# Kernel tuning notes

Hardware: AMD Instinct MI355X
Metric: run time of the kernel (lower is better)

## Reference

```python
import jax, jax.numpy as jnp
import numpy as np

# Expert output sizes per answer type: yes/no, number, other (VQA v2)
SIZES = [2, 482, 3129]
MAX_ANS = max(SIZES)  # 3129, padded output width
D_IN = 1024
D_HID = 1000
BATCH = 16384
N_TYPES = len(SIZES)


def setup_inputs() -> dict:
    key = jax.random.key(0)
    ks = jax.random.split(key, 2 + 4 * N_TYPES)
    inp = {
        "hidden_states": jax.random.normal(ks[0], (BATCH, D_IN), dtype=jnp.float32),
        "question_type_output": jax.random.normal(ks[1], (BATCH, N_TYPES), dtype=jnp.float32),
    }
    # Learned params for each expert MLP: Linear(1024->1000), Tanh, Linear(1000->n_e)
    for e, n_out in enumerate(SIZES):
        k1, k2, k3, k4 = ks[2 + 4 * e], ks[3 + 4 * e], ks[4 + 4 * e], ks[5 + 4 * e]
        inp[f"w1_{e}"] = jax.random.normal(k1, (D_IN, D_HID), dtype=jnp.float32) * 0.02
        inp[f"b1_{e}"] = jax.random.normal(k2, (D_HID,), dtype=jnp.float32) * 0.02
        inp[f"w2_{e}"] = jax.random.normal(k3, (D_HID, n_out), dtype=jnp.float32) * 0.02
        inp[f"b2_{e}"] = jax.random.normal(k4, (n_out,), dtype=jnp.float32) * 0.02
    return inp


def _expert(x, w1, b1, w2, b2):
    # Linear -> Dropout(eval: identity) -> Tanh -> Linear
    return jnp.tanh(x @ w1 + b1) @ w2 + b2


def reference(hidden_states, question_type_output,
              w1_0, b1_0, w2_0, b2_0,
              w1_1, b1_1, w2_1, b2_1,
              w1_2, b1_2, w2_2, b2_2):
    params = [(w1_0, b1_0, w2_0, b2_0),
              (w1_1, b1_1, w2_1, b2_1),
              (w1_2, b1_2, w2_2, b2_2)]
    # Route each sample to the expert of its argmax question type.
    pred = jnp.argmax(question_type_output, axis=1)  # [B] int
    out = jnp.zeros((hidden_states.shape[0], MAX_ANS), dtype=hidden_states.dtype)
    # Small fixed loop over N_TYPES experts (structurally distinct weights);
    # each expert runs batched over all samples, then a mask selects routed rows.
    for e, (w1, b1, w2, b2) in enumerate(params):
        o = _expert(hidden_states, w1, b1, w2, b2)          # [B, n_e]
        o = jnp.pad(o, ((0, 0), (0, MAX_ANS - o.shape[1])))  # zero-pad to [B, MAX]
        out = jnp.where((pred == e)[:, None], o, out)
    return out
```

## Files before the change

### kernel.cpp

```cpp
#include <hip/hip_runtime.h>

typedef __attribute__((ext_vector_type(8))) __bf16 bf16x8;
typedef __attribute__((ext_vector_type(4))) float f32x4;

constexpr int BATCH = 16384;
constexpr int DIN   = 1024;
constexpr int DHID  = 1000;
constexpr int MAXA  = 3129;
constexpr int MBMAX = 131;

constexpr size_t SZ_AP  = (size_t)MBMAX * 32 * 8192;
constexpr size_t SZ_HP  = SZ_AP;
constexpr size_t SZ_W1P = 3 * 8 * 32 * 8192;
constexpr size_t SZ_W2P = 30 * 32 * 8192;
constexpr size_t WS_HP  = 0;
constexpr size_t WS_W1P = WS_HP + SZ_HP;
constexpr size_t WS_W2P = WS_W1P + SZ_W1P;
constexpr size_t WS_CNT = WS_W2P + SZ_W2P;
constexpr size_t WS_IDX = WS_CNT + 1024;
constexpr size_t WS_AP  = WS_IDX + 3 * BATCH * 4;
constexpr size_t WS_NEED = WS_AP + SZ_AP;

constexpr int PA_BLK = 2096;
constexpr int PW1_BLK = 1536;
constexpr int PW2_BLK = 1920;

__device__ __forceinline__ ushort f2bf(float f) {
    return __builtin_bit_cast(ushort, (__bf16)f);
}

__device__ __forceinline__ void gload16(const void* g, void* l) {
    __builtin_amdgcn_global_load_lds((const __attribute__((address_space(1))) void*)g,
                                     (__attribute__((address_space(3))) void*)l, 16, 0, 0);
}

__global__ void zero_k(int* __restrict__ c) { if (threadIdx.x < 16) c[threadIdx.x] = 0; }

__global__ void route_k(const float* __restrict__ qt, int* __restrict__ counts,
                        int* __restrict__ idx) {
    int i = blockIdx.x * 256 + threadIdx.x;
    if (i >= BATCH) return;
    float a = qt[3 * i], b = qt[3 * i + 1], c = qt[3 * i + 2];
    int p = 0; float m = a;
    if (b > m) { m = b; p = 1; }
    if (c > m) { m = c; p = 2; }
    int pos = atomicAdd(&counts[p], 1);
    idx[p * BATCH + pos] = i;
}

__global__ void pack_all_k(const float* __restrict__ hs,
                           const float* __restrict__ w1_0, const float* __restrict__ w1_1,
                           const float* __restrict__ w1_2,
                           const float* __restrict__ w2_0, const float* __restrict__ w2_1,
                           const float* __restrict__ w2_2,
                           const int* __restrict__ counts, const int* __restrict__ idx,
                           ushort* __restrict__ Ap, ushort* __restrict__ W1p,
                           ushort* __restrict__ W2p) {
    const int b = blockIdx.x, tid = threadIdx.x;
    if (b < PA_BLK) {
        const int g = b * 256 + tid;
        const int m = g & 127, kt = (g >> 7) & 31, mb = g >> 12;
        const int c0 = counts[0], c1 = counts[1], c2 = counts[2];
        const int n0 = (c0 + 127) >> 7, n1 = (c1 + 127) >> 7, n2 = (c2 + 127) >> 7;
        if (mb >= n0 + n1 + n2) return;
        int e = 0, lm = mb, cnt = c0;
        if (lm >= n0) { lm -= n0; e = 1; cnt = c1; }
        if (e == 1 && lm >= n1) { lm -= n1; e = 2; cnt = c2; }
        int ri = lm * 128 + m; if (ri >= cnt) ri = cnt - 1;
        const float* row = hs + (size_t)idx[e * BATCH + ri] * DIN + kt * 32;
        ushort* dst = Ap + (size_t)(mb * 32 + kt) * 4096 + m * 8;
#pragma unroll
        for (int kc = 0; kc < 4; kc++) {
            float4 f0 = *reinterpret_cast<const float4*>(row + kc * 8);
            float4 f1 = *reinterpret_cast<const float4*>(row + kc * 8 + 4);
            union { ushort u[8]; int4 v; } p;
            p.u[0] = f2bf(f0.x); p.u[1] = f2bf(f0.y); p.u[2] = f2bf(f0.z); p.u[3] = f2bf(f0.w);
            p.u[4] = f2bf(f1.x); p.u[5] = f2bf(f1.y); p.u[6] = f2bf(f1.z); p.u[7] = f2bf(f1.w);
            *reinterpret_cast<int4*>(dst + kc * 1024) = p.v;
        }
    } else if (b < PA_BLK + PW1_BLK) {
        const int g = (b - PA_BLK) * 256 + tid;
        const int n = g & 127, kc = (g >> 7) & 3, kt = (g >> 9) & 31, nb = (g >> 14) & 7, e = g >> 17;
        const float* W = e == 0 ? w1_0 : e == 1 ? w1_1 : w1_2;
        const int nn = nb * 128 + n;
        union { ushort u[8]; int4 v; } p;
#pragma unroll
        for (int j = 0; j < 8; j++) {
            int k = kt * 32 + kc * 8 + j;
            float f = (nn < DHID) ? W[(size_t)k * DHID + nn] : 0.f;
            p.u[j] = f2bf(f);
        }
        *reinterpret_cast<int4*>(W1p + ((size_t)((e * 8 + nb) * 32 + kt)) * 4096 + (kc * 128 + n) * 8) = p.v;
    } else {
        const int g = (b - PA_BLK - PW1_BLK) * 256 + tid;
        const int n = g & 127, kc = (g >> 7) & 3, kt = (g >> 9) & 31, t = g >> 14;
        const int e = (t < 1) ? 0 : (t < 5) ? 1 : 2;
        const int nb = t - (e == 0 ? 0 : e == 1 ? 1 : 5);
        const int ne = e == 0 ? 2 : e == 1 ? 482 : MAXA;
        const float* W = e == 0 ? w2_0 : e == 1 ? w2_1 : w2_2;
        const int nn = nb * 128 + n;
        union { ushort u[8]; int4 v; } p;
#pragma unroll
        for (int j = 0; j < 8; j++) {
            int k = kt * 32 + kc * 8 + j;
            float f = (k < DHID && nn < ne) ? W[(size_t)k * ne + nn] : 0.f;
            p.u[j] = f2bf(f);
        }
        *reinterpret_cast<int4*>(W2p + ((size_t)(t * 32 + kt)) * 4096 + (kc * 128 + n) * 8) = p.v;
    }
}

#define STAGE(BUFO, KT)                                                         \
    {                                                                           \
        const char* as_ = Ag + (size_t)(KT) * 8192 + tid * 16;                  \
        gload16(as_, lds + (BUFO) + w * 1024);                                  \
        const char* bs_ = Bg + (size_t)(KT) * 8192 + tid * 16;                  \
        gload16(bs_, lds + (BUFO) + 8192 + w * 1024);                           \
    }

#define KLOOP()                                                                 \
    f32x4 acc[2][4] = {};                                                       \
    STAGE(0, 0)                                                                 \
    STAGE(16384, 1)                                                             \
    {                                                                           \
        int cur = 0;                                                            \
        for (int kt = 0; kt < 32; ++kt) {                                       \
            if (kt < 31) asm volatile("s_waitcnt vmcnt(2)" ::: "memory");       \
            else         asm volatile("s_waitcnt vmcnt(0)" ::: "memory");       \
            asm volatile("s_barrier" ::: "memory");                             \
            if (kt + 2 < 32) {                                                  \
                int nx = cur + 2; if (nx >= 3) nx -= 3;                         \
                STAGE(nx * 16384, kt + 2)                                       \
            }                                                                   \
            const char* base = lds + cur * 16384;                               \
            bf16x8 af[2], bfr[4];                                               \
            _Pragma("unroll")                                                   \
            for (int mi = 0; mi < 2; mi++)                                      \
                af[mi] = *reinterpret_cast<const bf16x8*>(                      \
                    base + kq4 * 2048 + (wm * 32 + mi * 16 + l15) * 16);        \
            _Pragma("unroll")                                                   \
            for (int ni = 0; ni < 4; ni++)                                      \
                bfr[ni] = *reinterpret_cast<const bf16x8*>(                     \
                    base + 8192 + kq4 * 2048 + (wn * 64 + ni * 16 + l15) * 16); \
            __builtin_amdgcn_s_setprio(1);                                      \
            _Pragma("unroll")                                                   \
            for (int mi = 0; mi < 2; mi++)                                      \
                _Pragma("unroll")                                               \
                for (int ni = 0; ni < 4; ni++)                                  \
                    acc[mi][ni] = __builtin_amdgcn_mfma_f32_16x16x32_bf16(      \
                        af[mi], bfr[ni], acc[mi][ni], 0, 0, 0);                 \
            __builtin_amdgcn_s_setprio(0);                                      \
            cur = cur + 1; if (cur == 3) cur = 0;                               \
        }                                                                       \
    }                                                                           \
    asm volatile("s_barrier" ::: "memory");

__global__ __launch_bounds__(512, 3)
void gemm1_k(const char* __restrict__ ApB, const char* __restrict__ W1pB,
             const float* __restrict__ b1_0, const float* __restrict__ b1_1,
             const float* __restrict__ b1_2,
             const int* __restrict__ counts, int* __restrict__ wq,
             char* __restrict__ HpB) {
    __shared__ __align__(16) char lds[49152];
    __shared__ int s_t;
    const int c0 = counts[0], c1 = counts[1], c2 = counts[2];
    const int n0 = (c0 + 127) >> 7, n1 = (c1 + 127) >> 7, n2 = (c2 + 127) >> 7;
    const int T = (n0 + n1 + n2) * 8;

    const int tid = threadIdx.x;
    const int lane = tid & 63, w = tid >> 6;
    const int wm = w >> 1, wn = w & 1;
    const int l15 = lane & 15, kq4 = lane >> 4;

    for (;;) {
        if (tid == 0) s_t = atomicAdd(wq, 1);
        __syncthreads();
        const int t = s_t;
        if (t >= T) break;

        const int mbG = t >> 3, nbk = t & 7;
        int e = 0, lm = mbG;
        if (lm >= n0) { lm -= n0; e = 1; }
        if (e == 1 && lm >= n1) { lm -= n1; e = 2; }
        const float* bias = e == 0 ? b1_0 : e == 1 ? b1_1 : b1_2;
        const char* Ag = ApB + (size_t)mbG * (32 * 8192);
        const char* Bg = W1pB + (size_t)((e * 8 + nbk) * 32) * 8192;

        KLOOP()

        ushort* img = (ushort*)lds;
#pragma unroll
        for (int mi = 0; mi < 2; mi++) {
            const int rb = wm * 32 + mi * 16 + kq4 * 4;
#pragma unroll
            for (int ni = 0; ni < 4; ni++) {
                const int nl = wn * 64 + ni * 16 + l15;
                const int ng = nbk * 128 + nl;
                const bool live = ng < DHID;
                const float bv = live ? bias[ng] : 0.f;
                const int ua = ((nl >> 5) * 4096 + ((nl >> 3) & 3) * 1024 + (nl & 6)) & ~1;
#pragma unroll
                for (int rg = 0; rg < 4; rg++) {
                    float vv = live ? tanhf(acc[mi][ni][rg] + bv) : 0.f;
                    float vo = __shfl_xor(vv, 1);
                    ushort lo = (l15 & 1) ? f2bf(vo) : f2bf(vv);
                    ushort hi = (l15 & 1) ? f2bf(vv) : f2bf(vo);
                    *reinterpret_cast<uint*>(img + ua + (rb + rg) * 8) =
                        (uint)lo | ((uint)hi << 16);
                }
            }
        }
        asm volatile("s_barrier" ::: "memory");
        char* hdst = HpB + ((size_t)mbG * 32 + nbk * 4) * 8192;
#pragma unroll
        for (int i2 = 0; i2 < 4; i2++) {
            const int s = tid + i2 * 512;
            *reinterpret_cast<int4*>(hdst + s * 16) =
                *reinterpret_cast<const int4*>(lds + s * 16);
        }
        asm volatile("s_barrier" ::: "memory");
    }
}

__global__ __launch_bounds__(512, 3)
void gemm2_k(const char* __restrict__ HpB, const char* __restrict__ W2pB,
             const float* __restrict__ b2_0, const float* __restrict__ b2_1,
             const float* __restrict__ b2_2,
             const int* __restrict__ counts, const int* __restrict__ idx,
             int* __restrict__ wq, int fallback, float* __restrict__ Out) {
    __shared__ __align__(16) char lds[49152];
    __shared__ int s_t;
    const int c0 = counts[0], c1 = counts[1], c2 = counts[2];
    int nb[3]  = {(c0 + 127) >> 7, (c1 + 127) >> 7, (c2 + 127) >> 7};
    int cc[3]  = {c0, c1, c2};
    const int nbn[3]  = {1, 4, 25};
    const int nz[3]   = {24, 21, 0};
    const int zst[3]  = {128, 512, 0};
    const int toff[3] = {0, 1, 5};
    const int nel[3]  = {2, 482, MAXA};
    const int Tc = nb[0] * 1 + nb[1] * 4 + nb[2] * 25;
    const int Tz = fallback ? (nb[0] * 24 + nb[1] * 21) : 0;
    const int T = Tc + Tz;

    const int tid = threadIdx.x;
    const int lane = tid & 63, w = tid >> 6;
    const int wm = w >> 1, wn = w & 1;
    const int l15 = lane & 15, kq4 = lane >> 4;

    for (;;) {
        if (tid == 0) s_t = atomicAdd(wq, 1);
        __syncthreads();
        const int t = s_t;
        if (t >= T) break;

        if (t < Tc) {
            int e = 0, r = t, mbG = 0;
            while (e < 2 && r >= nb[e] * nbn[e]) { r -= nb[e] * nbn[e]; mbG += nb[e]; ++e; }
            const int lm = r / nbn[e], nbk = r - lm * nbn[e];
            mbG += lm;
            const int cnt = cc[e], ne = nel[e];
            const float* bias = e == 0 ? b2_0 : e == 1 ? b2_1 : b2_2;
            const char* Ag = HpB + (size_t)mbG * (32 * 8192);
            const char* Bg = W2pB + (size_t)((toff[e] + nbk) * 32) * 8192;

            KLOOP()

            const int m0 = lm * 128;
            float* bf32 = (float*)lds;
            const int* ip = idx + e * BATCH;
#pragma unroll
            for (int h = 0; h < 2; h++) {
                if ((wm >> 1) == h) {
#pragma unroll
                    for (int mi = 0; mi < 2; mi++) {
                        const int rl = (wm & 1) * 32 + mi * 16 + kq4 * 4;
#pragma unroll
                        for (int ni = 0; ni < 4; ni++) {
                            const int nl = wn * 64 + ni * 16 + l15;
                            const int ncol = nbk * 128 + nl;
                            const bool live = ncol < ne;
                            const float bv = live ? bias[ncol] : 0.f;
#pragma unroll
                            for (int rg = 0; rg < 4; rg++)
                                bf32[(rl + rg) * 132 + nl] =
                                    live ? (acc[mi][ni][rg] + bv) : 0.f;
                        }
                    }
                }
                asm volatile("s_barrier" ::: "memory");
#pragma unroll
                for (int i2 = 0; i2 < 4; i2++) {
                    const int s = tid + i2 * 512;
                    const int rr = s >> 5, c4 = s & 31;
                    const int mrow = m0 + h * 64 + rr;
                    const int ncol0 = nbk * 128 + c4 * 4;
                    if (mrow < cnt && ncol0 < ne) {
                        const int orow = ip[mrow];
                        float4 val = *reinterpret_cast<const float4*>(bf32 + rr * 132 + c4 * 4);
                        float* op = Out + (size_t)orow * MAXA + ncol0;
                        if (ncol0 + 3 < MAXA) {
                            *reinterpret_cast<float4*>(op) = val;
                        } else {
                            if (ncol0 + 0 < MAXA) op[0] = val.x;
                            if (ncol0 + 1 < MAXA) op[1] = val.y;
                            if (ncol0 + 2 < MAXA) op[2] = val.z;
                            if (ncol0 + 3 < MAXA) op[3] = val.w;
                        }
                    }
                }
                asm volatile("s_barrier" ::: "memory");
            }
        } else {
            int e = 0, r = t - Tc;
            while (e < 2 && r >= nb[e] * nz[e]) { r -= nb[e] * nz[e]; ++e; }
            const int lm = r / nz[e], zc = r - lm * nz[e];
            const int cnt = cc[e];
            const int col0 = zst[e] + zc * 128;
            const int width = (MAXA - col0 < 128) ? (MAXA - col0) : 128;
            const int m0 = lm * 128;
            const int nrow = (cnt - m0 < 128) ? (cnt - m0) : 128;
            const int* rowp = idx + e * BATCH + m0;
            const float4 z4 = {0.f, 0.f, 0.f, 0.f};
            if (width == 128) {
                for (int s = tid; s < (nrow << 5); s += 512) {
                    const int rl = s >> 5, c4 = s & 31;
                    *reinterpret_cast<float4*>(Out + (size_t)rowp[rl] * MAXA + col0 + c4 * 4) = z4;
                }
            } else {
                const int f4 = width >> 2;
                for (int s = tid; s < nrow * f4; s += 512) {
                    const int rl = s / f4, c4 = s - rl * f4;
                    *reinterpret_cast<float4*>(Out + (size_t)rowp[rl] * MAXA + col0 + c4 * 4) = z4;
                }
                const int rem = width & 3;
                for (int s = tid; s < nrow * rem; s += 512) {
                    const int rl = s / rem, j = s - rl * rem;
                    Out[(size_t)rowp[rl] * MAXA + col0 + f4 * 4 + j] = 0.f;
                }
            }
            __syncthreads();
        }
    }
}

extern "C" void kernel_launch(void* const* d_in, const int* in_sizes, int n_in,
                              void* d_out, int out_size, void* d_ws, size_t ws_size,
                              hipStream_t stream) {
    const float* hs = (const float*)d_in[0];
    const float* qt = (const float*)d_in[1];
    const float* w1_0 = (const float*)d_in[2],  *b1_0 = (const float*)d_in[3];
    const float* w2_0 = (const float*)d_in[4],  *b2_0 = (const float*)d_in[5];
    const float* w1_1 = (const float*)d_in[6],  *b1_1 = (const float*)d_in[7];
    const float* w2_1 = (const float*)d_in[8],  *b2_1 = (const float*)d_in[9];
    const float* w1_2 = (const float*)d_in[10], *b1_2 = (const float*)d_in[11];
    const float* w2_2 = (const float*)d_in[12], *b2_2 = (const float*)d_in[13];

    char* ws = (char*)d_ws;
    ushort* Hp  = (ushort*)(ws + WS_HP);
    ushort* W1p = (ushort*)(ws + WS_W1P);
    ushort* W2p = (ushort*)(ws + WS_W2P);
    int* counts = (int*)(ws + WS_CNT);
    int* idx    = (int*)(ws + WS_IDX);
    const int fallback = (ws_size >= WS_NEED) ? 0 : 1;
    ushort* Ap = fallback ? (ushort*)((char*)d_out + ((size_t)out_size * 4 - SZ_AP))
                          : (ushort*)(ws + WS_AP);
    float* Out = (float*)d_out;

    zero_k<<<1, 64, 0, stream>>>(counts);
    route_k<<<64, 256, 0, stream>>>(qt, counts, idx);
    pack_all_k<<<PA_BLK + PW1_BLK + PW2_BLK, 256, 0, stream>>>(
        hs, w1_0, w1_1, w1_2, w2_0, w2_1, w2_2, counts, idx, Ap, W1p, W2p);
    gemm1_k<<<384, 512, 0, stream>>>((const char*)Ap, (const char*)W1p,
                                     b1_0, b1_1, b1_2, counts, counts + 8, (char*)Hp);
    gemm2_k<<<384, 512, 0, stream>>>((const char*)Hp, (const char*)W2p,
                                     b2_0, b2_1, b2_2, counts, idx, counts + 12,
                                     fallback, Out);
}
```

Baseline: 331.3 us.

## Replace LDS-staged 512-thread GEMM tiles with single-wave register-direct 64x64 tiles

Both GEMM kernels move from 512-thread workgroups that stage 128x128 tiles through triple-buffered LDS via global_load_lds to single-wavefront workgroups. Each wave computes a 64x64 tile and loads its A/B fragments directly from global memory into registers with double buffering. This removes LDS traffic and workgroup barriers and adds more parallel work items. The cost is lost inter-wave reuse in LDS, which means more global/L2 reads per FLOP. The gemm2 epilogue now writes scattered scalar outputs directly instead of coalesced float4 stores through LDS.

```diff
diff --git a/kernel.cpp b/kernel.cpp
--- a/kernel.cpp
+++ b/kernel.cpp
@@ -27,11 +27,6 @@
 
 __device__ __forceinline__ ushort f2bf(float f) {
     return __builtin_bit_cast(ushort, (__bf16)f);
-}
-
-__device__ __forceinline__ void gload16(const void* g, void* l) {
-    __builtin_amdgcn_global_load_lds((const __attribute__((address_space(1))) void*)g,
-                                     (__attribute__((address_space(3))) void*)l, 16, 0, 0);
 }
 
 __global__ void zero_k(int* __restrict__ c) { if (threadIdx.x < 16) c[threadIdx.x] = 0; }
@@ -110,95 +105,88 @@
     }
 }
 
-#define STAGE(BUFO, KT)                                                         \
+#define LD4(dst, P)                                                             \
     {                                                                           \
-        const char* as_ = Ag + (size_t)(KT) * 8192 + tid * 16;                  \
-        gload16(as_, lds + (BUFO) + w * 1024);                                  \
-        const char* bs_ = Bg + (size_t)(KT) * 8192 + tid * 16;                  \
-        gload16(bs_, lds + (BUFO) + 8192 + w * 1024);                           \
-    }
-
-#define KLOOP()                                                                 \
-    f32x4 acc[2][4] = {};                                                       \
-    STAGE(0, 0)                                                                 \
-    STAGE(16384, 1)                                                             \
+        dst[0] = *reinterpret_cast<const bf16x8*>((P));                         \
+        dst[1] = *reinterpret_cast<const bf16x8*>((P) + 256);                   \
+        dst[2] = *reinterpret_cast<const bf16x8*>((P) + 512);                   \
+        dst[3] = *reinterpret_cast<const bf16x8*>((P) + 768);                   \
+    }
+
+#define MM(A, B)                                                                \
     {                                                                           \
-        int cur = 0;                                                            \
-        for (int kt = 0; kt < 32; ++kt) {                                       \
-            if (kt < 31) asm volatile("s_waitcnt vmcnt(2)" ::: "memory");       \
-            else         asm volatile("s_waitcnt vmcnt(0)" ::: "memory");       \
-            asm volatile("s_barrier" ::: "memory");                             \
-            if (kt + 2 < 32) {                                                  \
-                int nx = cur + 2; if (nx >= 3) nx -= 3;                         \
-                STAGE(nx * 16384, kt + 2)                                       \
-            }                                                                   \
-            const char* base = lds + cur * 16384;                               \
-            bf16x8 af[2], bfr[4];                                               \
-            _Pragma("unroll")                                                   \
-            for (int mi = 0; mi < 2; mi++)                                      \
-                af[mi] = *reinterpret_cast<const bf16x8*>(                      \
-                    base + kq4 * 2048 + (wm * 32 + mi * 16 + l15) * 16);        \
+        __builtin_amdgcn_s_setprio(1);                                          \
+        _Pragma("unroll")                                                       \
+        for (int mi = 0; mi < 4; mi++)                                          \
             _Pragma("unroll")                                                   \
             for (int ni = 0; ni < 4; ni++)                                      \
-                bfr[ni] = *reinterpret_cast<const bf16x8*>(                     \
-                    base + 8192 + kq4 * 2048 + (wn * 64 + ni * 16 + l15) * 16); \
-            __builtin_amdgcn_s_setprio(1);                                      \
-            _Pragma("unroll")                                                   \
-            for (int mi = 0; mi < 2; mi++)                                      \
-                _Pragma("unroll")                                               \
-                for (int ni = 0; ni < 4; ni++)                                  \
-                    acc[mi][ni] = __builtin_amdgcn_mfma_f32_16x16x32_bf16(      \
-                        af[mi], bfr[ni], acc[mi][ni], 0, 0, 0);                 \
-            __builtin_amdgcn_s_setprio(0);                                      \
-            cur = cur + 1; if (cur == 3) cur = 0;                               \
+                acc[mi][ni] = __builtin_amdgcn_mfma_f32_16x16x32_bf16(          \
+                    A[mi], B[ni], acc[mi][ni], 0, 0, 0);                        \
+        __builtin_amdgcn_s_setprio(0);                                          \
+    }
+
+#define KLOOPW()                                                                \
+    f32x4 acc[4][4] = {};                                                       \
+    {                                                                           \
+        bf16x8 a0[4], b0[4], a1[4], b1[4];                                      \
+        const char* ap = Ag + aoff;                                             \
+        const char* bp = Bg + boff;                                             \
+        LD4(a0, ap) LD4(b0, bp)                                                 \
+        for (int kt = 0; kt < 32; kt += 2) {                                    \
+            LD4(a1, ap + 8192) LD4(b1, bp + 8192)                               \
+            MM(a0, b0)                                                          \
+            if (kt + 2 < 32) { LD4(a0, ap + 16384) LD4(b0, bp + 16384) }        \
+            MM(a1, b1)                                                          \
+            ap += 16384; bp += 16384;                                           \
         }                                                                       \
-    }                                                                           \
-    asm volatile("s_barrier" ::: "memory");
-
-__global__ __launch_bounds__(512, 3)
+    }
+
+__global__ __launch_bounds__(64, 2)
 void gemm1_k(const char* __restrict__ ApB, const char* __restrict__ W1pB,
              const float* __restrict__ b1_0, const float* __restrict__ b1_1,
              const float* __restrict__ b1_2,
              const int* __restrict__ counts, int* __restrict__ wq,
              char* __restrict__ HpB) {
-    __shared__ __align__(16) char lds[49152];
-    __shared__ int s_t;
+    __shared__ __align__(16) char lds[8192];
     const int c0 = counts[0], c1 = counts[1], c2 = counts[2];
     const int n0 = (c0 + 127) >> 7, n1 = (c1 + 127) >> 7, n2 = (c2 + 127) >> 7;
-    const int T = (n0 + n1 + n2) * 8;
-
-    const int tid = threadIdx.x;
-    const int lane = tid & 63, w = tid >> 6;
-    const int wm = w >> 1, wn = w & 1;
+    const int M2 = (n0 + n1 + n2) * 2;
+    const int T = M2 * 16;
+
+    const int lane = threadIdx.x;
     const int l15 = lane & 15, kq4 = lane >> 4;
 
     for (;;) {
-        if (tid == 0) s_t = atomicAdd(wq, 1);
-        __syncthreads();
-        const int t = s_t;
+        int t;
+        if (lane == 0) t = atomicAdd(wq, 1);
+        t = __shfl(t, 0);
         if (t >= T) break;
 
-        const int mbG = t >> 3, nbk = t & 7;
-        int e = 0, lm = mbG;
+        const int mt = t >> 4, nt = t & 15;
+        const int mb = mt >> 1, r0 = (mt & 1) * 64;
+        int e = 0, lm = mb;
         if (lm >= n0) { lm -= n0; e = 1; }
         if (e == 1 && lm >= n1) { lm -= n1; e = 2; }
         const float* bias = e == 0 ? b1_0 : e == 1 ? b1_1 : b1_2;
-        const char* Ag = ApB + (size_t)mbG * (32 * 8192);
-        const char* Bg = W1pB + (size_t)((e * 8 + nbk) * 32) * 8192;
-
-        KLOOP()
+        const char* Ag = ApB + (size_t)mb * (32 * 8192);
+        const char* Bg = W1pB + (size_t)((e * 8 + (nt >> 1)) * 32) * 8192;
+        const int c0l = (nt & 1) * 64;
+        const int aoff = kq4 * 2048 + (r0 + l15) * 16;
+        const int boff = kq4 * 2048 + (c0l + l15) * 16;
+
+        KLOOPW()
 
         ushort* img = (ushort*)lds;
 #pragma unroll
-        for (int mi = 0; mi < 2; mi++) {
-            const int rb = wm * 32 + mi * 16 + kq4 * 4;
+        for (int mi = 0; mi < 4; mi++) {
+            const int rb = mi * 16 + kq4 * 4;
 #pragma unroll
             for (int ni = 0; ni < 4; ni++) {
-                const int nl = wn * 64 + ni * 16 + l15;
-                const int ng = nbk * 128 + nl;
+                const int nl = ni * 16 + l15;
+                const int ng = nt * 64 + nl;
                 const bool live = ng < DHID;
                 const float bv = live ? bias[ng] : 0.f;
-                const int ua = ((nl >> 5) * 4096 + ((nl >> 3) & 3) * 1024 + (nl & 6)) & ~1;
+                const int ua = (nl >> 5) * 2048 + ((nl >> 3) & 3) * 512 + (nl & 6);
 #pragma unroll
                 for (int rg = 0; rg < 4; rg++) {
                     float vv = live ? tanhf(acc[mi][ni][rg] + bv) : 0.f;
@@ -210,105 +198,77 @@
                 }
             }
         }
-        asm volatile("s_barrier" ::: "memory");
-        char* hdst = HpB + ((size_t)mbG * 32 + nbk * 4) * 8192;
-#pragma unroll
-        for (int i2 = 0; i2 < 4; i2++) {
-            const int s = tid + i2 * 512;
-            *reinterpret_cast<int4*>(hdst + s * 16) =
-                *reinterpret_cast<const int4*>(lds + s * 16);
-        }
-        asm volatile("s_barrier" ::: "memory");
-    }
-}
-
-__global__ __launch_bounds__(512, 3)
+#pragma unroll
+        for (int p = 0; p < 8; p++) {
+            const int c = p >> 2, kc = p & 3;
+            char* dst = HpB + ((size_t)mb * 32 + nt * 2 + c) * 8192 + kc * 2048 + r0 * 16;
+            *reinterpret_cast<int4*>(dst + lane * 16) =
+                *reinterpret_cast<const int4*>(lds + p * 1024 + lane * 16);
+        }
+    }
+}
+
+__global__ __launch_bounds__(64, 2)
 void gemm2_k(const char* __restrict__ HpB, const char* __restrict__ W2pB,
              const float* __restrict__ b2_0, const float* __restrict__ b2_1,
              const float* __restrict__ b2_2,
              const int* __restrict__ counts, const int* __restrict__ idx,
              int* __restrict__ wq, int fallback, float* __restrict__ Out) {
-    __shared__ __align__(16) char lds[49152];
-    __shared__ int s_t;
     const int c0 = counts[0], c1 = counts[1], c2 = counts[2];
     int nb[3]  = {(c0 + 127) >> 7, (c1 + 127) >> 7, (c2 + 127) >> 7};
     int cc[3]  = {c0, c1, c2};
-    const int nbn[3]  = {1, 4, 25};
+    const int N2[3]   = {1, 8, 49};
     const int nz[3]   = {24, 21, 0};
     const int zst[3]  = {128, 512, 0};
     const int toff[3] = {0, 1, 5};
     const int nel[3]  = {2, 482, MAXA};
-    const int Tc = nb[0] * 1 + nb[1] * 4 + nb[2] * 25;
+    const int M2e[3]  = {nb[0] * 2, nb[1] * 2, nb[2] * 2};
+    const int Tc = M2e[0] * N2[0] + M2e[1] * N2[1] + M2e[2] * N2[2];
     const int Tz = fallback ? (nb[0] * 24 + nb[1] * 21) : 0;
     const int T = Tc + Tz;
 
-    const int tid = threadIdx.x;
-    const int lane = tid & 63, w = tid >> 6;
-    const int wm = w >> 1, wn = w & 1;
+    const int lane = threadIdx.x;
     const int l15 = lane & 15, kq4 = lane >> 4;
 
     for (;;) {
-        if (tid == 0) s_t = atomicAdd(wq, 1);
-        __syncthreads();
-        const int t = s_t;
+        int t;
+        if (lane == 0) t = atomicAdd(wq, 1);
+        t = __shfl(t, 0);
         if (t >= T) break;
 
         if (t < Tc) {
-            int e = 0, r = t, mbG = 0;
-            while (e < 2 && r >= nb[e] * nbn[e]) { r -= nb[e] * nbn[e]; mbG += nb[e]; ++e; }
-            const int lm = r / nbn[e], nbk = r - lm * nbn[e];
-            mbG += lm;
+            int e = 0, r = t, mb128base = 0;
+            while (e < 2 && r >= M2e[e] * N2[e]) { r -= M2e[e] * N2[e]; mb128base += nb[e]; ++e; }
+            const int lm2 = r / N2[e], nt = r - lm2 * N2[e];
+            const int mbG = mb128base + (lm2 >> 1), r0 = (lm2 & 1) * 64;
             const int cnt = cc[e], ne = nel[e];
             const float* bias = e == 0 ? b2_0 : e == 1 ? b2_1 : b2_2;
             const char* Ag = HpB + (size_t)mbG * (32 * 8192);
-            const char* Bg = W2pB + (size_t)((toff[e] + nbk) * 32) * 8192;
-
-            KLOOP()
-
-            const int m0 = lm * 128;
-            float* bf32 = (float*)lds;
+            const char* Bg = W2pB + (size_t)((toff[e] + (nt >> 1)) * 32) * 8192;
+            const int c0l = (nt & 1) * 64;
+            const int aoff = kq4 * 2048 + (r0 + l15) * 16;
+            const int boff = kq4 * 2048 + (c0l + l15) * 16;
+
+            KLOOPW()
+
+            const int m0 = lm2 * 64;
             const int* ip = idx + e * BATCH;
 #pragma unroll
-            for (int h = 0; h < 2; h++) {
-                if ((wm >> 1) == h) {
-#pragma unroll
-                    for (int mi = 0; mi < 2; mi++) {
-                        const int rl = (wm & 1) * 32 + mi * 16 + kq4 * 4;
+            for (int mi = 0; mi < 4; mi++) {
+#pragma unroll
+                for (int rg = 0; rg < 4; rg++) {
+                    const int rl = mi * 16 + kq4 * 4 + rg;
+                    const int mrow = m0 + rl;
+                    if (mrow < cnt) {
+                        const size_t obase = (size_t)ip[mrow] * MAXA;
 #pragma unroll
                         for (int ni = 0; ni < 4; ni++) {
-                            const int nl = wn * 64 + ni * 16 + l15;
-                            const int ncol = nbk * 128 + nl;
-                            const bool live = ncol < ne;
-                            const float bv = live ? bias[ncol] : 0.f;
-#pragma unroll
-                            for (int rg = 0; rg < 4; rg++)
-                                bf32[(rl + rg) * 132 + nl] =
-                                    live ? (acc[mi][ni][rg] + bv) : 0.f;
+                            const int ncol = nt * 64 + ni * 16 + l15;
+                            if (ncol < ne)
+                                Out[obase + ncol] = acc[mi][ni][rg] + bias[ncol];
                         }
                     }
                 }
-                asm volatile("s_barrier" ::: "memory");
-#pragma unroll
-                for (int i2 = 0; i2 < 4; i2++) {
-                    const int s = tid + i2 * 512;
-                    const int rr = s >> 5, c4 = s & 31;
-                    const int mrow = m0 + h * 64 + rr;
-                    const int ncol0 = nbk * 128 + c4 * 4;
-                    if (mrow < cnt && ncol0 < ne) {
-                        const int orow = ip[mrow];
-                        float4 val = *reinterpret_cast<const float4*>(bf32 + rr * 132 + c4 * 4);
-                        float* op = Out + (size_t)orow * MAXA + ncol0;
-                        if (ncol0 + 3 < MAXA) {
-                            *reinterpret_cast<float4*>(op) = val;
-                        } else {
-                            if (ncol0 + 0 < MAXA) op[0] = val.x;
-                            if (ncol0 + 1 < MAXA) op[1] = val.y;
-                            if (ncol0 + 2 < MAXA) op[2] = val.z;
-                            if (ncol0 + 3 < MAXA) op[3] = val.w;
-                        }
-                    }
-                }
-                asm volatile("s_barrier" ::: "memory");
             }
         } else {
             int e = 0, r = t - Tc;
@@ -322,23 +282,22 @@
             const int* rowp = idx + e * BATCH + m0;
             const float4 z4 = {0.f, 0.f, 0.f, 0.f};
             if (width == 128) {
-                for (int s = tid; s < (nrow << 5); s += 512) {
+                for (int s = lane; s < (nrow << 5); s += 64) {
                     const int rl = s >> 5, c4 = s & 31;
                     *reinterpret_cast<float4*>(Out + (size_t)rowp[rl] * MAXA + col0 + c4 * 4) = z4;
                 }
             } else {
                 const int f4 = width >> 2;
-                for (int s = tid; s < nrow * f4; s += 512) {
+                for (int s = lane; s < nrow * f4; s += 64) {
                     const int rl = s / f4, c4 = s - rl * f4;
                     *reinterpret_cast<float4*>(Out + (size_t)rowp[rl] * MAXA + col0 + c4 * 4) = z4;
                 }
                 const int rem = width & 3;
-                for (int s = tid; s < nrow * rem; s += 512) {
+                for (int s = lane; s < nrow * rem; s += 64) {
                     const int rl = s / rem, j = s - rl * rem;
                     Out[(size_t)rowp[rl] * MAXA + col0 + f4 * 4 + j] = 0.f;
                 }
             }
-            __syncthreads();
         }
     }
 }
@@ -370,9 +329,9 @@
     route_k<<<64, 256, 0, stream>>>(qt, counts, idx);
     pack_all_k<<<PA_BLK + PW1_BLK + PW2_BLK, 256, 0, stream>>>(
         hs, w1_0, w1_1, w1_2, w2_0, w2_1, w2_2, counts, idx, Ap, W1p, W2p);
-    gemm1_k<<<384, 512, 0, stream>>>((const char*)Ap, (const char*)W1p,
+    gemm1_k<<<2560, 64, 0, stream>>>((const char*)Ap, (const char*)W1p,
                                      b1_0, b1_1, b1_2, counts, counts + 8, (char*)Hp);
-    gemm2_k<<<384, 512, 0, stream>>>((const char*)Hp, (const char*)W2p,
+    gemm2_k<<<2560, 64, 0, stream>>>((const char*)Hp, (const char*)W2p,
                                      b2_0, b2_1, b2_2, counts, idx, counts + 12,
                                      fallback, Out);
 }
```

Result: slower. 402.7 us (+21.5%).
